# Kernel tuning notes

Measured on AMD Instinct MI355X. Metric: run time of the kernel, lower is better.

The kernel has to match this reference:

```python
import jax, jax.numpy as jnp
import numpy as np

D_MODEL = 1024
N_HEADS = 16
HEAD = D_MODEL // N_HEADS  # 64


def setup_inputs() -> dict:
    key = jax.random.key(0)
    ks = jax.random.split(key, 6)
    B, T = 2, 2048
    x = jax.random.normal(ks[0], (B, T, D_MODEL), dtype=jnp.float32)
    s_in = 1.0 / np.sqrt(HEAD)
    # per-head projections: Linear(head_size -> d_model), no bias. Stored as [H, head, d_model].
    Wq = jax.random.normal(ks[1], (N_HEADS, HEAD, D_MODEL), dtype=jnp.float32) * s_in
    Wk = jax.random.normal(ks[2], (N_HEADS, HEAD, D_MODEL), dtype=jnp.float32) * s_in
    Wv = jax.random.normal(ks[3], (N_HEADS, HEAD, D_MODEL), dtype=jnp.float32) * s_in
    # output projection: Linear(H*d_model -> d_model) with bias
    Wo = jax.random.normal(ks[4], (N_HEADS * D_MODEL, D_MODEL), dtype=jnp.float32) / np.sqrt(N_HEADS * D_MODEL)
    bo = jax.random.normal(ks[5], (D_MODEL,), dtype=jnp.float32) * 0.01
    return {"x": x, "Wq": Wq, "Wk": Wk, "Wv": Wv, "Wo": Wo, "bo": bo}


def reference(x, Wq, Wk, Wv, Wo, bo):
    B, T, _ = x.shape
    # split into per-head slices: [B, H, T, head]
    xh = x.reshape(B, T, N_HEADS, HEAD).transpose(0, 2, 1, 3)
    q = jnp.einsum("bhtd,hdm->bhtm", xh, Wq)  # [B,H,T,d_model]
    k = jnp.einsum("bhtd,hdm->bhtm", xh, Wk)
    v = jnp.einsum("bhtd,hdm->bhtm", xh, Wv)
    # scale uses D = head input dim (= HEAD), per the original code
    scores = jnp.einsum("bhtm,bhsm->bhts", q, k) / jnp.sqrt(jnp.asarray(HEAD, x.dtype))
    weights = jax.nn.softmax(scores, axis=-1)
    vb = jnp.einsum("bhts,bhsm->bhtm", weights, v)  # [B,H,T,d_model]
    cat = vb.transpose(0, 2, 1, 3).reshape(B, T, N_HEADS * D_MODEL)
    return cat @ Wo + bo
```

## Files before the change

### kernel.cpp

```cpp
#include <hip/hip_runtime.h>
#include <math.h>

typedef unsigned u32;
typedef unsigned short u16;
typedef __attribute__((ext_vector_type(8))) __bf16 bf16x8;
typedef __attribute__((ext_vector_type(4))) float f32x4;

#define DEVI __device__ __forceinline__

DEVI u16 f2bf(float f) {
    u32 u = __builtin_bit_cast(u32, f);
    u += 0x7fffu + ((u >> 16) & 1u);
    return (u16)(u >> 16);
}

DEVI u32 packbf(float a, float b) {
    u32 ua = __builtin_bit_cast(u32, a) + 0x8000u;
    u32 ub = __builtin_bit_cast(u32, b) + 0x8000u;
    return (ua >> 16) | (ub & 0xffff0000u);
}

DEVI bf16x8 ldsf(const u16* p) { return *(const bf16x8*)p; }

DEVI f32x4 mfma16(bf16x8 a, bf16x8 b, f32x4 c) {
    return __builtin_amdgcn_mfma_f32_16x16x32_bf16(a, b, c, 0, 0, 0);
}

#if __has_builtin(__builtin_amdgcn_exp2f)
DEVI float fexp2(float x) { return __builtin_amdgcn_exp2f(x); }
#else
DEVI float fexp2(float x) { return exp2f(x); }
#endif

__global__ __launch_bounds__(256) void k_pw(const float* __restrict__ x,
                                            const float* __restrict__ Wq, const float* __restrict__ Wk,
                                            const float* __restrict__ Wv, const float* __restrict__ Wo,
                                            u16* __restrict__ xswz, u16* __restrict__ xt2,
                                            u16* __restrict__ mtg, u16* __restrict__ W2) {
    __shared__ __align__(16) char SM[36864];
    const int tid = threadIdx.x;
    const int id = blockIdx.x;
    const int rr = tid >> 2, c16 = (tid & 3) * 16;

    if (id < 272) {
        u16* LA0 = (u16*)SM;
        u16* LB0 = (u16*)(SM + 9216);
        u16* LA1 = (u16*)(SM + 18432);
        u16* LB1 = (u16*)(SM + 27648);
        const int w = tid >> 6, lane = tid & 63, g = lane >> 4, ln = lane & 15;
        f32x4 acc[4] = {};
        float4 pa0[4], pb0[4], pa1[4], pb1[4];

        auto mm = [&](const u16* LAp, const u16* LBp) {
#pragma unroll
            for (int ks = 0; ks < 2; ks++) {
                bf16x8 bb = ldsf(LBp + (w * 16 + ln) * 72 + ks * 32 + g * 8);
#pragma unroll
                for (int mt = 0; mt < 4; mt++) {
                    bf16x8 a = ldsf(LAp + (mt * 16 + ln) * 72 + ks * 32 + g * 8);
                    acc[mt] = mfma16(a, bb, acc[mt]);
                }
            }
        };
        auto bar = [&]() {
            asm volatile("s_waitcnt lgkmcnt(0)" ::: "memory");
            __builtin_amdgcn_s_barrier();
            __builtin_amdgcn_sched_barrier(0);
        };

        if (id >= 256) {
            const int h = id - 256;
            auto loadT = [&](int t, float4* pa, float4* pb) {
                const float4* sa = (const float4*)(Wk + (h * 64 + rr) * 1024 + t * 64 + c16);
                const float4* sb = (const float4*)(Wq + (h * 64 + rr) * 1024 + t * 64 + c16);
#pragma unroll
                for (int j = 0; j < 4; j++) { pa[j] = sa[j]; pb[j] = sb[j]; }
            };
            auto cvtW = [&](u16* LAp, u16* LBp, float4* pa, float4* pb) {
                union { uint4 q[2]; u16 s[16]; } ua, ub;
#pragma unroll
                for (int j = 0; j < 4; j++) {
                    ua.s[j*4+0]=f2bf(pa[j].x); ua.s[j*4+1]=f2bf(pa[j].y); ua.s[j*4+2]=f2bf(pa[j].z); ua.s[j*4+3]=f2bf(pa[j].w);
                    ub.s[j*4+0]=f2bf(pb[j].x); ub.s[j*4+1]=f2bf(pb[j].y); ub.s[j*4+2]=f2bf(pb[j].z); ub.s[j*4+3]=f2bf(pb[j].w);
                }
                *(uint4*)(LAp + rr * 72 + c16) = ua.q[0]; *(uint4*)(LAp + rr * 72 + c16 + 8) = ua.q[1];
                *(uint4*)(LBp + rr * 72 + c16) = ub.q[0]; *(uint4*)(LBp + rr * 72 + c16 + 8) = ub.q[1];
            };
            loadT(0, pa0, pb0);
            cvtW(LA0, LB0, pa0, pb0);
            loadT(1, pa1, pb1);
            bar();
            for (int kb = 0; kb < 16; kb += 2) {
                if (kb + 2 < 16) loadT(kb + 2, pa0, pb0);
                mm(LA0, LB0);
                cvtW(LA1, LB1, pa1, pb1);
                bar();
                if (kb + 3 < 16) loadT(kb + 3, pa1, pb1);
                mm(LA1, LB1);
                if (kb + 2 < 16) cvtW(LA0, LB0, pa0, pb0);
                bar();
            }
#pragma unroll
            for (int mt = 0; mt < 4; mt++)
#pragma unroll
                for (int r = 0; r < 4; r++)
                    mtg[h * 4096 + (mt * 16 + g * 4 + r) * 64 + w * 16 + ln] =
                        f2bf(acc[mt][r] * 0.18033688011112f);
        } else {
            const int h = id >> 4, n0 = (id & 15) * 64;
            auto loadT = [&](int t, float4* pa, float4* pb) {
                const float4* sa = (const float4*)(Wo + (h * 1024 + t * 64 + rr) * 1024 + n0 + c16);
                const float4* sb = (const float4*)(Wv + (h * 64 + rr) * 1024 + t * 64 + c16);
#pragma unroll
                for (int j = 0; j < 4; j++) { pa[j] = sa[j]; pb[j] = sb[j]; }
            };
            auto cvtW = [&](u16* LAp, u16* LBp, float4* pa, float4* pb) {
                union { uint4 q[2]; u16 s[16]; } ub;
#pragma unroll
                for (int j = 0; j < 4; j++) {
                    ub.s[j*4+0]=f2bf(pb[j].x); ub.s[j*4+1]=f2bf(pb[j].y); ub.s[j*4+2]=f2bf(pb[j].z); ub.s[j*4+3]=f2bf(pb[j].w);
                }
                *(uint4*)(LBp + rr * 72 + c16) = ub.q[0]; *(uint4*)(LBp + rr * 72 + c16 + 8) = ub.q[1];
#pragma unroll
                for (int j = 0; j < 4; j++) {
                    LAp[(c16 + j * 4 + 0) * 72 + rr] = f2bf(pa[j].x);
                    LAp[(c16 + j * 4 + 1) * 72 + rr] = f2bf(pa[j].y);
                    LAp[(c16 + j * 4 + 2) * 72 + rr] = f2bf(pa[j].z);
                    LAp[(c16 + j * 4 + 3) * 72 + rr] = f2bf(pa[j].w);
                }
            };
            loadT(0, pa0, pb0);
            cvtW(LA0, LB0, pa0, pb0);
            loadT(1, pa1, pb1);
            bar();
            for (int kb = 0; kb < 16; kb += 2) {
                if (kb + 2 < 16) loadT(kb + 2, pa0, pb0);
                mm(LA0, LB0);
                cvtW(LA1, LB1, pa1, pb1);
                bar();
                if (kb + 3 < 16) loadT(kb + 3, pa1, pb1);
                mm(LA1, LB1);
                if (kb + 2 < 16) cvtW(LA0, LB0, pa0, pb0);
                bar();
            }
            int d = w * 16 + ln;
#pragma unroll
            for (int mt = 0; mt < 4; mt++)
#pragma unroll
                for (int r = 0; r < 4; r++) {
                    int n = n0 + mt * 16 + g * 4 + r;
                    W2[h * 65536 + n * 64 + (((d >> 3) ^ (n & 7)) << 3) + (d & 7)] = f2bf(acc[mt][r]);
                }
        }
    } else {
        const int pid = id - 272;
        const int kt = pid & 31, h = (pid >> 5) & 15, b = pid >> 9, bh = b * 16 + h;
        float* T = (float*)SM;
        int t = kt * 64 + rr;
        const float4* gx = (const float4*)(x + (b * 2048 + t) * 1024 + h * 64 + c16);
        float4 f[4];
#pragma unroll
        for (int j = 0; j < 4; j++) f[j] = gx[j];
#pragma unroll
        for (int j = 0; j < 4; j++) {
            T[rr * 65 + c16 + j * 4 + 0] = f[j].x; T[rr * 65 + c16 + j * 4 + 1] = f[j].y;
            T[rr * 65 + c16 + j * 4 + 2] = f[j].z; T[rr * 65 + c16 + j * 4 + 3] = f[j].w;
        }
        {
            union { uint4 q[2]; u16 s[16]; } u;
#pragma unroll
            for (int j = 0; j < 4; j++) {
                u.s[j * 4 + 0] = f2bf(f[j].x); u.s[j * 4 + 1] = f2bf(f[j].y);
                u.s[j * 4 + 2] = f2bf(f[j].z); u.s[j * 4 + 3] = f2bf(f[j].w);
            }
            u16* dst = xswz + (bh * 2048 + t) * 64;
            int c0 = (tid & 3) * 2, sw = rr & 7;
            *(uint4*)(dst + ((c0 ^ sw) << 3))       = u.q[0];
            *(uint4*)(dst + (((c0 + 1) ^ sw) << 3)) = u.q[1];
        }
        __syncthreads();
        int dd = tid >> 2, t4 = (tid & 3) * 16;
        union { uint2 d2[4]; u16 s[16]; } ou;
#pragma unroll
        for (int j = 0; j < 16; j++) ou.s[j] = f2bf(T[(t4 + j) * 65 + dd]);
        u16* dst = xt2 + bh * 131072 + kt * 4096 + dd * 64;
        const int nt0 = t4 >> 4;
        const int cb = (nt0 >> 1) * 4;
        const int off = (nt0 & 1) * 4;
        const int sw = dd & 7;
#pragma unroll
        for (int g4 = 0; g4 < 4; g4++) {
            int c = cb + g4;
            *(uint2*)(dst + ((c ^ sw) << 3) + off) = ou.d2[g4];
        }
    }
}

__global__ __launch_bounds__(256, 2) void k_attn(const u16* __restrict__ xswz, const u16* __restrict__ xt2,
                                                 const u16* __restrict__ mtg, u16* __restrict__ U2) {
    __shared__ __align__(16) u16 smem[20480];
    u16* KB = smem;
    u16* VB = smem + 8192;

    const int tid = threadIdx.x;
    const int w = tid >> 6, lane = tid & 63, g = lane >> 4, ln = lane & 15, ln7 = lane & 7;
    const int kvh = w & 1, qh2 = w >> 1;
    const int nid = (blockIdx.x & 7) * 64 + (blockIdx.x >> 3);
    const int qtb = nid & 15, h = (nid >> 4) & 15, b = nid >> 8, bh = b * 16 + h;
    const u16* xs = xswz + bh * 131072;
    const u16* xv = xt2 + bh * 131072;

    bf16x8 qf[4][2];
    {
        u16* LM  = smem;
        u16* LXQ = smem + 4608;
        {
            int r4 = tid >> 2, c4 = (tid & 3) * 2;
            const uint4* gm = (const uint4*)(mtg + h * 4096 + r4 * 64);
            uint4 m0 = gm[c4], m1 = gm[c4 + 1];
            *(uint4*)(LM + r4 * 72 + c4 * 8)     = m0;
            *(uint4*)(LM + r4 * 72 + c4 * 8 + 8) = m1;
            int r2 = tid >> 1, c2 = (tid & 1) * 4;
            const uint4* gx = (const uint4*)(xs + (qtb * 128 + r2) * 64);
            uint4 x0 = gx[c2], x1 = gx[c2 + 1], x2 = gx[c2 + 2], x3 = gx[c2 + 3];
            *(uint4*)(LXQ + r2 * 72 + c2 * 8)      = x0;
            *(uint4*)(LXQ + r2 * 72 + c2 * 8 + 8)  = x1;
            *(uint4*)(LXQ + r2 * 72 + c2 * 8 + 16) = x2;
            *(uint4*)(LXQ + r2 * 72 + c2 * 8 + 24) = x3;
        }
        __syncthreads();
        f32x4 acc[2][4] = {};
#pragma unroll
        for (int qh = 0; qh < 2; qh++) {
            int row = qh * 64 + w * 16 + ln;
#pragma unroll
            for (int ks = 0; ks < 2; ks++) {
                bf16x8 a = ldsf(LXQ + row * 72 + (((ks * 4 + g) ^ ln7) << 3));
#pragma unroll
                for (int nt = 0; nt < 4; nt++) {
                    bf16x8 bb = ldsf(LM + (nt * 16 + ln) * 72 + ks * 32 + g * 8);
                    acc[qh][nt] = mfma16(a, bb, acc[qh][nt]);
                }
            }
        }
        __syncthreads();
#pragma unroll
        for (int qh = 0; qh < 2; qh++) {
            u16* QLw = smem + qh * 4608 + w * 1152;
#pragma unroll
            for (int nt = 0; nt < 4; nt++)
#pragma unroll
                for (int r = 0; r < 4; r++)
                    QLw[(g * 4 + r) * 72 + nt * 16 + ln] = f2bf(acc[qh][nt][r]);
        }
        __syncthreads();
#pragma unroll
        for (int qt = 0; qt < 4; qt++) {
            const u16* QLr = smem + qh2 * 4608 + qt * 1152;
            qf[qt][0] = ldsf(QLr + ln * 72 + g * 8);
            qf[qt][1] = ldsf(QLr + ln * 72 + 32 + g * 8);
        }
        __syncthreads();
    }

    {
        const uint4* gk = (const uint4*)xs;
        const uint4* gv = (const uint4*)xv;
        uint4 k0 = gk[tid], k1 = gk[tid + 256], v0 = gv[tid], v1 = gv[tid + 256];
        uint4* lk = (uint4*)KB;
        uint4* lv = (uint4*)VB;
        lk[tid] = k0; lk[tid + 256] = k1; lv[tid] = v0; lv[tid + 256] = v1;
    }
    asm volatile("s_waitcnt lgkmcnt(0)" ::: "memory");
    __builtin_amdgcn_s_barrier();
    __builtin_amdgcn_sched_barrier(0);

    float lrow[4] = {0.f, 0.f, 0.f, 0.f};
    f32x4 o[4][4] = {};

#pragma unroll 2
    for (int kt = 0; kt < 32; ++kt) {
        const int cur = (kt & 1) << 12;
        const u16* KL = KB + cur;
        const u16* VL = VB + cur;

        uint4 kr0, kr1, vr0, vr1;
        if (kt + 1 < 32) {
            const uint4* gk = (const uint4*)(xs + (kt + 1) * 4096);
            const uint4* gv = (const uint4*)(xv + (kt + 1) * 4096);
            kr0 = gk[tid]; kr1 = gk[tid + 256]; vr0 = gv[tid]; vr1 = gv[tid + 256];
        }

        f32x4 s[2][4] = {};
        __builtin_amdgcn_s_setprio(1);
#pragma unroll
        for (int ks = 0; ks < 2; ks++) {
#pragma unroll
            for (int nt = 0; nt < 2; nt++) {
                bf16x8 a = ldsf(KL + ((kvh * 2 + nt) * 16 + ln) * 64 + (((ks * 4 + g) ^ ln7) << 3));
#pragma unroll
                for (int qt = 0; qt < 4; qt++)
                    s[nt][qt] = mfma16(a, qf[qt][ks], s[nt][qt]);
            }
        }
        __builtin_amdgcn_s_setprio(0);

        u32 pk[2][4][2];
#pragma unroll
        for (int qt = 0; qt < 4; qt++) {
            float ts = 0.f;
#pragma unroll
            for (int nt = 0; nt < 2; nt++) {
                float p0 = fexp2(s[nt][qt][0]), p1 = fexp2(s[nt][qt][1]);
                float p2 = fexp2(s[nt][qt][2]), p3 = fexp2(s[nt][qt][3]);
                pk[nt][qt][0] = packbf(p0, p1);
                pk[nt][qt][1] = packbf(p2, p3);
                ts += (p0 + p1) + (p2 + p3);
            }
            lrow[qt] += ts;
        }

        __builtin_amdgcn_s_setprio(1);
        {
            union { u32 u[4]; bf16x8 v; } pf[4];
#pragma unroll
            for (int qt = 0; qt < 4; qt++) {
                pf[qt].u[0] = pk[0][qt][0];
                pf[qt].u[1] = pk[0][qt][1];
                pf[qt].u[2] = pk[1][qt][0];
                pf[qt].u[3] = pk[1][qt][1];
            }
#pragma unroll
            for (int dt = 0; dt < 4; dt++) {
                bf16x8 a = ldsf(VL + (dt * 16 + ln) * 64 + (((kvh * 4 + g) ^ ln7) << 3));
#pragma unroll
                for (int qt = 0; qt < 4; qt++)
                    o[dt][qt] = mfma16(a, pf[qt].v, o[dt][qt]);
            }
        }
        __builtin_amdgcn_s_setprio(0);

        if (kt + 1 < 32) {
            const int nxt = cur ^ 4096;
            uint4* lk = (uint4*)(KB + nxt);
            uint4* lv = (uint4*)(VB + nxt);
            lk[tid] = kr0; lk[tid + 256] = kr1; lv[tid] = vr0; lv[tid + 256] = vr1;
        }
        asm volatile("s_waitcnt lgkmcnt(0)" ::: "memory");
        __builtin_amdgcn_s_barrier();
        __builtin_amdgcn_sched_barrier(0);
    }

#pragma unroll
    for (int qt = 0; qt < 4; qt++) {
        lrow[qt] += __shfl_xor(lrow[qt], 16, 64);
        lrow[qt] += __shfl_xor(lrow[qt], 32, 64);
    }
    float* LO = (float*)smem;
    if (kvh == 1) {
        float* B = LO + qh2 * 4290;
#pragma unroll
        for (int dt = 0; dt < 4; dt++)
#pragma unroll
            for (int qt = 0; qt < 4; qt++)
#pragma unroll
                for (int r = 0; r < 4; r++)
                    B[(dt * 16 + g * 4 + r) * 66 + qt * 16 + ln] = o[dt][qt][r];
        if (g == 0) {
#pragma unroll
            for (int qt = 0; qt < 4; qt++)
                B[64 * 66 + qt * 16 + ln] = lrow[qt];
        }
    }
    __syncthreads();
    if (kvh == 0) {
        float* B = LO + qh2 * 4290;
#pragma unroll
        for (int dt = 0; dt < 4; dt++)
#pragma unroll
            for (int qt = 0; qt < 4; qt++)
#pragma unroll
                for (int r = 0; r < 4; r++)
                    o[dt][qt][r] += B[(dt * 16 + g * 4 + r) * 66 + qt * 16 + ln];
#pragma unroll
        for (int qt = 0; qt < 4; qt++) {
            float lr = lrow[qt] + B[64 * 66 + qt * 16 + ln];
            float inv = 1.0f / lr;
            int t = b * 2048 + qtb * 128 + qh2 * 64 + qt * 16 + ln;
#pragma unroll
            for (int dt = 0; dt < 4; dt++) {
                ushort4 vv;
                vv.x = f2bf(o[dt][qt][0] * inv); vv.y = f2bf(o[dt][qt][1] * inv);
                vv.z = f2bf(o[dt][qt][2] * inv); vv.w = f2bf(o[dt][qt][3] * inv);
                int c = dt * 2 + (g >> 1);
                int pos = c ^ (t & 7);
                *(ushort4*)(U2 + h * 262144 + t * 64 + pos * 8 + (g & 1) * 4) = vv;
            }
        }
    }
}

__global__ __launch_bounds__(512) void k_out(const u16* __restrict__ U2, const u16* __restrict__ W2,
                                             const float* __restrict__ bo, float* __restrict__ out) {
    __shared__ __align__(16) u16 SMu[32768];
    const int tid = threadIdx.x;
    const int w = tid >> 6, lane = tid & 63, g = lane >> 4, ln = lane & 15;
    const int nid = (blockIdx.x & 7) * 32 + (blockIdx.x >> 3);
    const int n0 = (nid & 7) * 128, r0 = (nid >> 3) * 128;
    const int wr = (w >> 2) * 64, wc = (w & 3) * 32;
    f32x4 acc[4][2] = {};
    uint4 ar[2], br[2];

    {
        const uint4* ga = (const uint4*)(U2 + r0 * 64);
        const uint4* gb = (const uint4*)(W2 + n0 * 64);
        ar[0] = ga[tid]; ar[1] = ga[tid + 512];
        br[0] = gb[tid]; br[1] = gb[tid + 512];
        ((uint4*)SMu)[tid] = ar[0]; ((uint4*)SMu)[tid + 512] = ar[1];
        ((uint4*)(SMu + 16384))[tid] = br[0]; ((uint4*)(SMu + 16384))[tid + 512] = br[1];
    }
    asm volatile("s_waitcnt lgkmcnt(0)" ::: "memory");
    __builtin_amdgcn_s_barrier();
    __builtin_amdgcn_sched_barrier(0);

    for (int kb = 0; kb < 16; kb++) {
        const int cu = (kb & 1) << 13;
        if (kb + 1 < 16) {
            const uint4* ga = (const uint4*)(U2 + (kb + 1) * 262144 + r0 * 64);
            const uint4* gb = (const uint4*)(W2 + (kb + 1) * 65536 + n0 * 64);
            ar[0] = ga[tid]; ar[1] = ga[tid + 512];
            br[0] = gb[tid]; br[1] = gb[tid + 512];
        }
        const u16* AL = SMu + cu;
        const u16* BL = SMu + 16384 + cu;
#pragma unroll
        for (int ks = 0; ks < 2; ks++) {
            bf16x8 af[4], bfr[2];
#pragma unroll
            for (int mt = 0; mt < 4; mt++) {
                int rr = wr + mt * 16 + ln;
                af[mt] = ldsf(AL + rr * 64 + (((ks * 4 + g) ^ (rr & 7)) << 3));
            }
#pragma unroll
            for (int nt = 0; nt < 2; nt++) {
                int rr = wc + nt * 16 + ln;
                bfr[nt] = ldsf(BL + rr * 64 + (((ks * 4 + g) ^ (rr & 7)) << 3));
            }
#pragma unroll
            for (int mt = 0; mt < 4; mt++)
#pragma unroll
                for (int nt = 0; nt < 2; nt++)
                    acc[mt][nt] = mfma16(af[mt], bfr[nt], acc[mt][nt]);
        }
        if (kb + 1 < 16) {
            const int nx = cu ^ 8192;
            uint4* la = (uint4*)(SMu + nx);
            uint4* lb = (uint4*)(SMu + 16384 + nx);
            la[tid] = ar[0]; la[tid + 512] = ar[1];
            lb[tid] = br[0]; lb[tid + 512] = br[1];
        }
        asm volatile("s_waitcnt lgkmcnt(0)" ::: "memory");
        __builtin_amdgcn_s_barrier();
        __builtin_amdgcn_sched_barrier(0);
    }

    float* Wp = (float*)SMu + w * 576;
    const int coff = (lane & 7) * 4;
    const float4 b4 = *(const float4*)(bo + n0 + wc + coff);
#pragma unroll
    for (int mt = 0; mt < 4; mt++) {
#pragma unroll
        for (int nt = 0; nt < 2; nt++)
#pragma unroll
            for (int r = 0; r < 4; r++)
                Wp[(g * 4 + r) * 36 + nt * 16 + ln] = acc[mt][nt][r];
        asm volatile("s_waitcnt lgkmcnt(0)" ::: "memory");
#pragma unroll
        for (int i = 0; i < 2; i++) {
            int row = (lane >> 3) + 8 * i;
            float4 v = *(const float4*)(Wp + row * 36 + coff);
            v.x += b4.x; v.y += b4.y; v.z += b4.z; v.w += b4.w;
            *(float4*)(out + (r0 + wr + mt * 16 + row) * 1024 + n0 + wc + coff) = v;
        }
    }
}

extern "C" void kernel_launch(void* const* d_in, const int* in_sizes, int n_in,
                              void* d_out, int out_size, void* d_ws, size_t ws_size,
                              hipStream_t stream) {
    const float* x  = (const float*)d_in[0];
    const float* Wq = (const float*)d_in[1];
    const float* Wk = (const float*)d_in[2];
    const float* Wv = (const float*)d_in[3];
    const float* Wo = (const float*)d_in[4];
    const float* bo = (const float*)d_in[5];
    float* out = (float*)d_out;

    char* ws = (char*)d_ws;
    u16* xswz = (u16*)(ws);
    u16* mtg  = (u16*)(ws + 8388608);
    u16* xt2  = (u16*)(ws + 8519680);
    u16* W2   = (u16*)(ws + 16908288);
    u16* U2   = (u16*)(ws + 19005440);

    k_pw<<<1296, 256, 0, stream>>>(x, Wq, Wk, Wv, Wo, xswz, xt2, mtg, W2);
    k_attn<<<512, 256, 0, stream>>>(xswz, xt2, mtg, U2);
    k_out<<<256, 512, 0, stream>>>(U2, W2, bo, out);
}
```

Before: 200.0 us.

## Split attention work across 8 waves per block, halving per-wave query tiles

The attention kernel now launches 512 threads (8 waves) per block instead of 256. Each wave handles 32 query rows instead of 64, so Q fragments, score tiles and output accumulators are halved. Each thread loads one uint4 each of K and V per tile instead of two. This lowers register pressure and raises the number of resident waves to hide latency. In exchange, each K/V fragment read from LDS feeds fewer MFMAs, and the per-tile barrier now synchronizes more waves.

```diff
diff --git a/kernel.cpp b/kernel.cpp
--- a/kernel.cpp
+++ b/kernel.cpp
@@ -196,7 +196,7 @@
     }
 }
 
-__global__ __launch_bounds__(256, 2) void k_attn(const u16* __restrict__ xswz, const u16* __restrict__ xt2,
+__global__ __launch_bounds__(512, 4) void k_attn(const u16* __restrict__ xswz, const u16* __restrict__ xt2,
                                                  const u16* __restrict__ mtg, u16* __restrict__ U2) {
     __shared__ __align__(16) u16 smem[20480];
     u16* KB = smem;
@@ -204,59 +204,52 @@
 
     const int tid = threadIdx.x;
     const int w = tid >> 6, lane = tid & 63, g = lane >> 4, ln = lane & 15, ln7 = lane & 7;
-    const int kvh = w & 1, qh2 = w >> 1;
+    const int kvh = w & 1, qq = w >> 1;
     const int nid = (blockIdx.x & 7) * 64 + (blockIdx.x >> 3);
     const int qtb = nid & 15, h = (nid >> 4) & 15, b = nid >> 8, bh = b * 16 + h;
     const u16* xs = xswz + bh * 131072;
     const u16* xv = xt2 + bh * 131072;
 
-    bf16x8 qf[4][2];
+    bf16x8 qf[2][2];
     {
         u16* LM  = smem;
         u16* LXQ = smem + 4608;
         {
-            int r4 = tid >> 2, c4 = (tid & 3) * 2;
+            int r4 = tid >> 3, c4 = tid & 7;
             const uint4* gm = (const uint4*)(mtg + h * 4096 + r4 * 64);
-            uint4 m0 = gm[c4], m1 = gm[c4 + 1];
-            *(uint4*)(LM + r4 * 72 + c4 * 8)     = m0;
-            *(uint4*)(LM + r4 * 72 + c4 * 8 + 8) = m1;
-            int r2 = tid >> 1, c2 = (tid & 1) * 4;
+            uint4 m0 = gm[c4];
+            *(uint4*)(LM + r4 * 72 + c4 * 8) = m0;
+            int r2 = tid >> 2, c2 = (tid & 3) * 2;
             const uint4* gx = (const uint4*)(xs + (qtb * 128 + r2) * 64);
-            uint4 x0 = gx[c2], x1 = gx[c2 + 1], x2 = gx[c2 + 2], x3 = gx[c2 + 3];
-            *(uint4*)(LXQ + r2 * 72 + c2 * 8)      = x0;
-            *(uint4*)(LXQ + r2 * 72 + c2 * 8 + 8)  = x1;
-            *(uint4*)(LXQ + r2 * 72 + c2 * 8 + 16) = x2;
-            *(uint4*)(LXQ + r2 * 72 + c2 * 8 + 24) = x3;
+            uint4 x0 = gx[c2], x1 = gx[c2 + 1];
+            *(uint4*)(LXQ + r2 * 72 + c2 * 8)     = x0;
+            *(uint4*)(LXQ + r2 * 72 + c2 * 8 + 8) = x1;
         }
         __syncthreads();
-        f32x4 acc[2][4] = {};
-#pragma unroll
-        for (int qh = 0; qh < 2; qh++) {
-            int row = qh * 64 + w * 16 + ln;
-#pragma unroll
-            for (int ks = 0; ks < 2; ks++) {
-                bf16x8 a = ldsf(LXQ + row * 72 + (((ks * 4 + g) ^ ln7) << 3));
-#pragma unroll
-                for (int nt = 0; nt < 4; nt++) {
-                    bf16x8 bb = ldsf(LM + (nt * 16 + ln) * 72 + ks * 32 + g * 8);
-                    acc[qh][nt] = mfma16(a, bb, acc[qh][nt]);
-                }
+        f32x4 acc[4] = {};
+        const int row = w * 16 + ln;
+#pragma unroll
+        for (int ks = 0; ks < 2; ks++) {
+            bf16x8 a = ldsf(LXQ + row * 72 + (((ks * 4 + g) ^ ln7) << 3));
+#pragma unroll
+            for (int nt = 0; nt < 4; nt++) {
+                bf16x8 bb = ldsf(LM + (nt * 16 + ln) * 72 + ks * 32 + g * 8);
+                acc[nt] = mfma16(a, bb, acc[nt]);
             }
         }
         __syncthreads();
-#pragma unroll
-        for (int qh = 0; qh < 2; qh++) {
-            u16* QLw = smem + qh * 4608 + w * 1152;
+        {
+            u16* QLw = smem + w * 1152;
 #pragma unroll
             for (int nt = 0; nt < 4; nt++)
 #pragma unroll
                 for (int r = 0; r < 4; r++)
-                    QLw[(g * 4 + r) * 72 + nt * 16 + ln] = f2bf(acc[qh][nt][r]);
+                    QLw[(g * 4 + r) * 72 + nt * 16 + ln] = f2bf(acc[nt][r]);
         }
         __syncthreads();
 #pragma unroll
-        for (int qt = 0; qt < 4; qt++) {
-            const u16* QLr = smem + qh2 * 4608 + qt * 1152;
+        for (int qt = 0; qt < 2; qt++) {
+            const u16* QLr = smem + (qq * 2 + qt) * 1152;
             qf[qt][0] = ldsf(QLr + ln * 72 + g * 8);
             qf[qt][1] = ldsf(QLr + ln * 72 + 32 + g * 8);
         }
@@ -264,19 +257,15 @@
     }
 
     {
-        const uint4* gk = (const uint4*)xs;
-        const uint4* gv = (const uint4*)xv;
-        uint4 k0 = gk[tid], k1 = gk[tid + 256], v0 = gv[tid], v1 = gv[tid + 256];
-        uint4* lk = (uint4*)KB;
-        uint4* lv = (uint4*)VB;
-        lk[tid] = k0; lk[tid + 256] = k1; lv[tid] = v0; lv[tid + 256] = v1;
+        uint4 k0 = ((const uint4*)xs)[tid], v0 = ((const uint4*)xv)[tid];
+        ((uint4*)KB)[tid] = k0; ((uint4*)VB)[tid] = v0;
     }
     asm volatile("s_waitcnt lgkmcnt(0)" ::: "memory");
     __builtin_amdgcn_s_barrier();
     __builtin_amdgcn_sched_barrier(0);
 
-    float lrow[4] = {0.f, 0.f, 0.f, 0.f};
-    f32x4 o[4][4] = {};
+    float lrow[2] = {0.f, 0.f};
+    f32x4 o[4][2] = {};
 
 #pragma unroll 2
     for (int kt = 0; kt < 32; ++kt) {
@@ -284,14 +273,13 @@
         const u16* KL = KB + cur;
         const u16* VL = VB + cur;
 
-        uint4 kr0, kr1, vr0, vr1;
+        uint4 kr0, vr0;
         if (kt + 1 < 32) {
-            const uint4* gk = (const uint4*)(xs + (kt + 1) * 4096);
-            const uint4* gv = (const uint4*)(xv + (kt + 1) * 4096);
-            kr0 = gk[tid]; kr1 = gk[tid + 256]; vr0 = gv[tid]; vr1 = gv[tid + 256];
-        }
-
-        f32x4 s[2][4] = {};
+            kr0 = ((const uint4*)(xs + (kt + 1) * 4096))[tid];
+            vr0 = ((const uint4*)(xv + (kt + 1) * 4096))[tid];
+        }
+
+        f32x4 s[2][2] = {};
         __builtin_amdgcn_s_setprio(1);
 #pragma unroll
         for (int ks = 0; ks < 2; ks++) {
@@ -299,15 +287,15 @@
             for (int nt = 0; nt < 2; nt++) {
                 bf16x8 a = ldsf(KL + ((kvh * 2 + nt) * 16 + ln) * 64 + (((ks * 4 + g) ^ ln7) << 3));
 #pragma unroll
-                for (int qt = 0; qt < 4; qt++)
+                for (int qt = 0; qt < 2; qt++)
                     s[nt][qt] = mfma16(a, qf[qt][ks], s[nt][qt]);
             }
         }
         __builtin_amdgcn_s_setprio(0);
 
-        u32 pk[2][4][2];
-#pragma unroll
-        for (int qt = 0; qt < 4; qt++) {
+        u32 pk[2][2][2];
+#pragma unroll
+        for (int qt = 0; qt < 2; qt++) {
             float ts = 0.f;
 #pragma unroll
             for (int nt = 0; nt < 2; nt++) {
@@ -322,9 +310,9 @@
 
         __builtin_amdgcn_s_setprio(1);
         {
-            union { u32 u[4]; bf16x8 v; } pf[4];
-#pragma unroll
-            for (int qt = 0; qt < 4; qt++) {
+            union { u32 u[4]; bf16x8 v; } pf[2];
+#pragma unroll
+            for (int qt = 0; qt < 2; qt++) {
                 pf[qt].u[0] = pk[0][qt][0];
                 pf[qt].u[1] = pk[0][qt][1];
                 pf[qt].u[2] = pk[1][qt][0];
@@ -334,7 +322,7 @@
             for (int dt = 0; dt < 4; dt++) {
                 bf16x8 a = ldsf(VL + (dt * 16 + ln) * 64 + (((kvh * 4 + g) ^ ln7) << 3));
 #pragma unroll
-                for (int qt = 0; qt < 4; qt++)
+                for (int qt = 0; qt < 2; qt++)
                     o[dt][qt] = mfma16(a, pf[qt].v, o[dt][qt]);
             }
         }
@@ -342,9 +330,8 @@
 
         if (kt + 1 < 32) {
             const int nxt = cur ^ 4096;
-            uint4* lk = (uint4*)(KB + nxt);
-            uint4* lv = (uint4*)(VB + nxt);
-            lk[tid] = kr0; lk[tid + 256] = kr1; lv[tid] = vr0; lv[tid + 256] = vr1;
+            ((uint4*)(KB + nxt))[tid] = kr0;
+            ((uint4*)(VB + nxt))[tid] = vr0;
         }
         asm volatile("s_waitcnt lgkmcnt(0)" ::: "memory");
         __builtin_amdgcn_s_barrier();
@@ -352,41 +339,41 @@
     }
 
 #pragma unroll
-    for (int qt = 0; qt < 4; qt++) {
+    for (int qt = 0; qt < 2; qt++) {
         lrow[qt] += __shfl_xor(lrow[qt], 16, 64);
         lrow[qt] += __shfl_xor(lrow[qt], 32, 64);
     }
     float* LO = (float*)smem;
     if (kvh == 1) {
-        float* B = LO + qh2 * 4290;
+        float* B = LO + qq * 2210;
 #pragma unroll
         for (int dt = 0; dt < 4; dt++)
 #pragma unroll
-            for (int qt = 0; qt < 4; qt++)
+            for (int qt = 0; qt < 2; qt++)
 #pragma unroll
                 for (int r = 0; r < 4; r++)
-                    B[(dt * 16 + g * 4 + r) * 66 + qt * 16 + ln] = o[dt][qt][r];
+                    B[(dt * 16 + g * 4 + r) * 34 + qt * 16 + ln] = o[dt][qt][r];
         if (g == 0) {
 #pragma unroll
-            for (int qt = 0; qt < 4; qt++)
-                B[64 * 66 + qt * 16 + ln] = lrow[qt];
+            for (int qt = 0; qt < 2; qt++)
+                B[64 * 34 + qt * 16 + ln] = lrow[qt];
         }
     }
     __syncthreads();
     if (kvh == 0) {
-        float* B = LO + qh2 * 4290;
+        float* B = LO + qq * 2210;
 #pragma unroll
         for (int dt = 0; dt < 4; dt++)
 #pragma unroll
-            for (int qt = 0; qt < 4; qt++)
+            for (int qt = 0; qt < 2; qt++)
 #pragma unroll
                 for (int r = 0; r < 4; r++)
-                    o[dt][qt][r] += B[(dt * 16 + g * 4 + r) * 66 + qt * 16 + ln];
-#pragma unroll
-        for (int qt = 0; qt < 4; qt++) {
-            float lr = lrow[qt] + B[64 * 66 + qt * 16 + ln];
+                    o[dt][qt][r] += B[(dt * 16 + g * 4 + r) * 34 + qt * 16 + ln];
+#pragma unroll
+        for (int qt = 0; qt < 2; qt++) {
+            float lr = lrow[qt] + B[64 * 34 + qt * 16 + ln];
             float inv = 1.0f / lr;
-            int t = b * 2048 + qtb * 128 + qh2 * 64 + qt * 16 + ln;
+            int t = b * 2048 + qtb * 128 + qq * 32 + qt * 16 + ln;
 #pragma unroll
             for (int dt = 0; dt < 4; dt++) {
                 ushort4 vv;
@@ -504,6 +491,6 @@
     u16* U2   = (u16*)(ws + 19005440);
 
     k_pw<<<1296, 256, 0, stream>>>(x, Wq, Wk, Wv, Wo, xswz, xt2, mtg, W2);
-    k_attn<<<512, 256, 0, stream>>>(xswz, xt2, mtg, U2);
+    k_attn<<<512, 512, 0, stream>>>(xswz, xt2, mtg, U2);
     k_out<<<256, 512, 0, stream>>>(U2, W2, bo, out);
 }
```

Result: no change. 201.1 us (+0.6%).
